# Kernel optimization log

Measured on AMD Instinct MI355X. Metric: run time of the kernel, lower is better.

Reference implementation:

```python
import jax, jax.numpy as jnp
from jax import lax
import numpy as np

TAU = 1.0          # epoch buffer = 0 -> tau_init * decay^0 = 1.0
NEG = -1.0e9
K_HOP = 2
MAX_CLUSTERS = 16
SIZE_MAX = 8
SIZE_MIN = 1
THRESH = 0.95
EPS = 1e-8


def _gumbel_hard(key, logits, m):
    # torch: logits*mask + (1-mask)*-1e9; gumbel noise; softmax; straight-through one-hot
    mf = m.astype(logits.dtype)
    ml = logits * mf + (1.0 - mf) * NEG
    u = jax.random.uniform(key, logits.shape, dtype=logits.dtype)
    g = -jnp.log(-jnp.log(u + EPS) + EPS)
    soft = jax.nn.softmax((ml + g) / TAU, axis=-1)
    idx = jnp.argmax(soft, axis=-1)
    hard = jax.nn.one_hot(idx, logits.shape[-1], dtype=logits.dtype)
    return hard + soft - lax.stop_gradient(soft), idx


def _k_hop(adj, seed_idx, m):
    # vectorized BFS via masked bmm, fixed K_HOP iterations
    N = adj.shape[1]
    seed = jax.nn.one_hot(seed_idx, N, dtype=bool)
    reach, cur = seed, seed
    for _ in range(K_HOP):
        nb = (jnp.einsum('bn,bnm->bm', cur.astype(adj.dtype), adj) > 0) & m
        new = nb & (~reach)
        reach = reach | nb
        cur = new
    return reach


def _topk_gumbel(key, logits, k, m):
    # iterative hard gumbel selection of up to k nodes per batch (k: [B] int)
    sel = jnp.zeros_like(logits)
    remaining = m
    for step in range(SIZE_MAX - SIZE_MIN):
        key, sk = jax.random.split(key)
        active = (step < k) & remaining.any(-1)
        step_mask = remaining & active[:, None]
        s, _ = _gumbel_hard(sk, logits, step_mask)
        sel = sel + s * active[:, None].astype(sel.dtype)
        remaining = remaining & ~(lax.stop_gradient(s) > 0.5)
    return sel


def _gru_seq(hist, h0, Wih, Whh, bih, bhh):
    # torch nn.GRU cell math, scan over time; hist [B,T,D], h0 [B,H]
    H = h0.shape[-1]
    def step(h, xt):
        gi = xt @ Wih.T + bih
        gh = h @ Whh.T + bhh
        r = jax.nn.sigmoid(gi[:, :H] + gh[:, :H])
        z = jax.nn.sigmoid(gi[:, H:2 * H] + gh[:, H:2 * H])
        n = jnp.tanh(gi[:, 2 * H:] + r * gh[:, 2 * H:])
        return (1.0 - z) * n + z * h, None
    h_final, _ = lax.scan(step, h0, jnp.swapaxes(hist, 0, 1))
    return h_final


def _forward(x, adj, mask, sel_w1, sel_b1, sel_w2, sel_b2,
             size_w1, size_b1, size_w2, size_b2,
             gru_wih, gru_whh, gru_bih, gru_bhh, init_w, init_b):
    B, N, D = x.shape
    H = init_w.shape[0]
    maskf = mask.astype(x.dtype)
    total = maskf.sum(-1)                                   # [B]
    x_mean = (x * maskf[:, :, None]).sum(1) / (total[:, None] + EPS)
    ctx_hidden = x_mean @ init_w.T + init_b                 # [B,H]
    global_ctx = ctx_hidden
    assignment = jnp.zeros((B, N, MAX_CLUSTERS), x.dtype)
    assigned = jnp.zeros((B, N), bool)
    history = []
    key = jax.random.key(42)
    size_range = jnp.arange(SIZE_MAX - SIZE_MIN + 1)
    for c in range(MAX_CLUSTERS):
        # gradient-safe early termination: mask contributions instead of breaking
        pct = assignment.sum((1, 2)) / (total + EPS)
        active = (pct < THRESH) & (total > 0)
        avail = mask & (~assigned)
        # selection MLP on [x, context]
        sel_in = jnp.concatenate(
            [x, jnp.broadcast_to(global_ctx[:, None, :], (B, N, H))], -1)
        h1 = jax.nn.relu(sel_in @ sel_w1.T + sel_b1)
        logits = (h1 @ sel_w2.T + sel_b2)[..., 0]           # [B,N]
        key, k1, k2, k3 = jax.random.split(key, 4)
        seed_sel, seed_idx = _gumbel_hard(k1, logits, avail)
        seed_feat = jnp.einsum('bn,bnd->bd', seed_sel, x)
        khop = _k_hop(adj, seed_idx, avail)
        candidates = khop & avail
        max_possible = jnp.minimum(candidates.sum(-1), SIZE_MAX)
        # cluster-size prediction
        size_in = jnp.concatenate(
            [seed_feat, global_ctx, max_possible.astype(x.dtype)[:, None]], -1)
        sh = jax.nn.relu(size_in @ size_w1.T + size_b1)
        size_logits = sh @ size_w2.T + size_b2              # [B,8]
        valid_ranges = jnp.clip(max_possible - SIZE_MIN + 1, 1, size_logits.shape[-1])
        range_mask = size_range[None, :] < valid_ranges[:, None]
        size_sel, _ = _gumbel_hard(k2, size_logits, range_mask)
        sizes = jnp.argmax(size_sel, -1) + SIZE_MIN         # [B]
        seed_oh = jax.nn.one_hot(seed_idx, N, dtype=bool)
        extra = _topk_gumbel(k3, logits, sizes - 1, candidates & (~seed_oh))
        cluster_sel = (seed_sel + extra) * active.astype(x.dtype)[:, None]
        assignment = assignment.at[:, :, c].set(cluster_sel)
        assigned = assigned | (lax.stop_gradient(cluster_sel) > 0.5)
        # gradient-safe cluster embedding (mean over selected nodes)
        csize = jnp.maximum(lax.stop_gradient(cluster_sel).sum(-1), 1.0)
        emb = jnp.einsum('bn,bnd->bd', cluster_sel, x) / csize[:, None]
        emb = emb * active.astype(x.dtype)[:, None]
        history.append(emb)
        # update_context_safe: rerun GRU on full history from current hidden
        hist = jnp.stack(history, 1)                        # [B,t+1,D]
        ctx_hidden = _gru_seq(hist, ctx_hidden, gru_wih, gru_whh, gru_bih, gru_bhh)
        global_ctx = ctx_hidden
    return assignment


def setup_inputs() -> dict:
    key = jax.random.key(0)
    ks = jax.random.split(key, 16)
    B, N, D, H = 32, 512, 128, 128
    x = jax.random.normal(ks[0], (B, N, D), jnp.float32)
    a = (jax.random.uniform(ks[1], (B, N, N)) < 0.02).astype(jnp.float32)
    adj = jnp.maximum(a, jnp.swapaxes(a, 1, 2))             # symmetric binary contacts
    mask = jnp.ones((B, N), bool)
    s = 0.05
    p = lambda k, sh: jax.random.normal(k, sh, jnp.float32) * s
    return dict(
        x=x, adj=adj, mask=mask,
        sel_w1=p(ks[2], (H, D + H)), sel_b1=p(ks[3], (H,)),
        sel_w2=p(ks[4], (1, H)), sel_b2=p(ks[5], (1,)),
        size_w1=p(ks[6], (H, D + H + 1)), size_b1=p(ks[7], (H,)),
        size_w2=p(ks[8], (SIZE_MAX, H)), size_b2=p(ks[9], (SIZE_MAX,)),
        gru_wih=p(ks[10], (3 * H, D)), gru_whh=p(ks[11], (3 * H, H)),
        gru_bih=p(ks[12], (3 * H,)), gru_bhh=p(ks[13], (3 * H,)),
        init_w=p(ks[14], (H, D)), init_b=p(ks[15], (H,)))


def reference(x, adj, mask, sel_w1, sel_b1, sel_w2, sel_b2,
              size_w1, size_b1, size_w2, size_b2,
              gru_wih, gru_whh, gru_bih, gru_bhh, init_w, init_b):
    return _forward(x, adj, mask, sel_w1, sel_b1, sel_w2, sel_b2,
                    size_w1, size_b1, size_w2, size_b2,
                    gru_wih, gru_whh, gru_bih, gru_bhh, init_w, init_b)
```

## Files before the change

kernel.cpp:

```cpp
#include <hip/hip_runtime.h>
#include <stdint.h>


#define NBATCH 32
#define NNODE  512
#define NDIM   128
#define NHID   128
#define NCLUS  16
#define NEGV   (-1.0e9f)
#define EPSF   (1e-8f)

struct KeyPack {
  uint32_t k1[NCLUS][2];
  uint32_t k2[NCLUS][2];
  uint32_t sk[NCLUS][7][2];
};

__host__ __device__ inline void tf2x32(uint32_t k0, uint32_t k1,
                                       uint32_t x0, uint32_t x1,
                                       uint32_t& o0, uint32_t& o1) {
  uint32_t k2 = k0 ^ k1 ^ 0x1BD11BDAu;
#define TFR(r) { x0 += x1; x1 = (x1 << (r)) | (x1 >> (32 - (r))); x1 ^= x0; }
  x0 += k0; x1 += k1;
  TFR(13) TFR(15) TFR(26) TFR(6)
  x0 += k1; x1 += k2 + 1u;
  TFR(17) TFR(29) TFR(16) TFR(24)
  x0 += k2; x1 += k0 + 2u;
  TFR(13) TFR(15) TFR(26) TFR(6)
  x0 += k0; x1 += k1 + 3u;
  TFR(17) TFR(29) TFR(16) TFR(24)
  x0 += k1; x1 += k2 + 4u;
  TFR(13) TFR(15) TFR(26) TFR(6)
  x0 += k2; x1 += k0 + 5u;
#undef TFR
  o0 = x0; o1 = x1;
}

__device__ __forceinline__ float jax_uniform(uint32_t k0, uint32_t k1, uint32_t j) {
  uint32_t a, b;
  tf2x32(k0, k1, 0u, j, a, b);
  uint32_t bits = a ^ b;
  return __uint_as_float((bits >> 9) | 0x3F800000u) - 1.0f;
}

__device__ __forceinline__ float gumb(float u) {
  return -logf(-logf(u + EPSF) + EPSF);
}

__device__ __forceinline__ float sigmf(float v) { return 1.0f / (1.0f + expf(-v)); }


__global__ void k_transpose(const float* __restrict__ gwih,
                            const float* __restrict__ gwhh,
                            const float* __restrict__ selw1, const float* __restrict__ szw1,
                            const float* __restrict__ initw,
                            float4* __restrict__ Wi3, float4* __restrict__ W3,
                            float* __restrict__ W1cT, float* __restrict__ szW1T,
                            float* __restrict__ initWT) {
  int t = blockIdx.x * blockDim.x + threadIdx.x;
  if (t < 32 * 384) {
    int i = t % 384, j4 = t / 384;
    const float* si = gwih + i * 128 + j4 * 4;
    Wi3[t] = make_float4(si[0], si[1], si[2], si[3]);
    const float* sh = gwhh + i * 128 + j4 * 4;
    W3[t]  = make_float4(sh[0], sh[1], sh[2], sh[3]);
  }
  if (t < 128 * 128) {
    int j = t >> 7, hh = t & 127;
    W1cT[t]   = selw1[hh * 256 + 128 + j];
    initWT[t] = initw[hh * 128 + j];
  }
  if (t < 257 * 128) {
    int j = t >> 7, i = t & 127;
    szW1T[t] = szw1[i * 257 + j];
  }
}

__global__ void k_adjbits(const float* __restrict__ adj, uint8_t* __restrict__ adjb8) {
  int t = blockIdx.x * blockDim.x + threadIdx.x;
  if (t >= NBATCH * NNODE * 64) return;
  const float4* p = (const float4*)adj + (size_t)t * 2;
  float4 a = p[0], b = p[1];
  uint32_t m = (a.x > 0.f ? 1u : 0u) | (a.y > 0.f ? 2u : 0u)
             | (a.z > 0.f ? 4u : 0u) | (a.w > 0.f ? 8u : 0u)
             | (b.x > 0.f ? 16u : 0u) | (b.y > 0.f ? 32u : 0u)
             | (b.z > 0.f ? 64u : 0u) | (b.w > 0.f ? 128u : 0u);
  adjb8[t] = (uint8_t)m;
}

__global__ __launch_bounds__(512)
void k_xw1(const float* __restrict__ x, const float* __restrict__ selw1,
           float* __restrict__ xw1T) {
  const int b = blockIdx.x >> 3;
  const int n0 = (blockIdx.x & 7) * 64;
  __shared__ float xs[64][NDIM + 1];
  for (int i = threadIdx.x; i < 64 * NDIM; i += 512) {
    int n = i >> 7, d = i & 127;
    xs[n][d] = x[((size_t)b * NNODE + n0 + n) * NDIM + d];
  }
  __syncthreads();
  for (int p = threadIdx.x; p < 64 * NHID; p += 512) {
    int h = p >> 6, n = p & 63;
    const float* wr = selw1 + h * 256;
    float a0 = 0.f, a1 = 0.f, a2 = 0.f, a3 = 0.f;
#pragma unroll 8
    for (int d = 0; d < NDIM; d += 4) {
      a0 = fmaf(xs[n][d + 0], wr[d + 0], a0);
      a1 = fmaf(xs[n][d + 1], wr[d + 1], a1);
      a2 = fmaf(xs[n][d + 2], wr[d + 2], a2);
      a3 = fmaf(xs[n][d + 3], wr[d + 3], a3);
    }
    xw1T[((size_t)b * NHID + h) * NNODE + n0 + n] = (a0 + a1) + (a2 + a3);
  }
}


#define MV384_PARTIALS(WP4, V4, PART)                                        \
  {                                                                          \
    const float4 cv0 = (V4)[wid * 4 + 0], cv1 = (V4)[wid * 4 + 1];           \
    const float4 cv2 = (V4)[wid * 4 + 2], cv3 = (V4)[wid * 4 + 3];           \
    _Pragma("unroll")                                                        \
    for (int m = 0; m < 6; m++) {                                            \
      const int row = lane + 64 * m;                                         \
      float4 w0 = (WP4)[row], w1 = (WP4)[384 + row];                         \
      float4 w2 = (WP4)[768 + row], w3v = (WP4)[1152 + row];                 \
      float pa = w0.x * cv0.x, pb = w0.y * cv0.y;                            \
      pa = fmaf(w0.z, cv0.z, pa);  pb = fmaf(w0.w, cv0.w, pb);               \
      pa = fmaf(w1.x, cv1.x, pa);  pb = fmaf(w1.y, cv1.y, pb);               \
      pa = fmaf(w1.z, cv1.z, pa);  pb = fmaf(w1.w, cv1.w, pb);               \
      pa = fmaf(w2.x, cv2.x, pa);  pb = fmaf(w2.y, cv2.y, pb);               \
      pa = fmaf(w2.z, cv2.z, pa);  pb = fmaf(w2.w, cv2.w, pb);               \
      pa = fmaf(w3v.x, cv3.x, pa); pb = fmaf(w3v.y, cv3.y, pb);              \
      pa = fmaf(w3v.z, cv3.z, pa); pb = fmaf(w3v.w, cv3.w, pb);              \
      (PART)[wid * 384 + row] = pa + pb;                                     \
    }                                                                        \
  }

__global__ __launch_bounds__(512)
void k_main(const float* __restrict__ x,
            const float* __restrict__ selb1, const float* __restrict__ selw2,
            const float* __restrict__ selb2,
            const float* __restrict__ szb1, const float* __restrict__ szw2,
            const float* __restrict__ szb2,
            const float* __restrict__ gbih, const float* __restrict__ gbhh,
            const float* __restrict__ initb,
            const float* __restrict__ xw1T, const uint32_t* __restrict__ adjb,
            const float4* __restrict__ Wi3, const float4* __restrict__ W3,
            const float* __restrict__ W1cT, const float* __restrict__ szW1T,
            const float* __restrict__ initWT,
            float* __restrict__ out, KeyPack kp)
{
  const int b = blockIdx.x;
  const int t = threadIdx.x;
  const int lane = t & 63, wid = t >> 6;

  __shared__ __align__(16) float4 resW[6144];
  __shared__ __align__(16) float gic[NCLUS][3 * NHID];
  __shared__ __align__(16) float partf[6144];
  __shared__ __align__(16) float gbhh_s[384];
  __shared__ __align__(16) float ctxb[NHID];
  __shared__ __align__(16) float ctxterm[NHID];
  __shared__ __align__(16) float cat256[2 * NHID];
  __shared__ __align__(16) float embs[NDIM];
  __shared__ __align__(16) float h1s[NHID];
  __shared__ __align__(16) float xm[NHID];
  __shared__ __align__(16) float selw2s[NHID];
  __shared__ float slog[8];
  __shared__ int   ibox[4];
  __shared__ uint32_t availw[16];
  __shared__ uint32_t curm[16];
  __shared__ uint32_t selm[16];

#pragma unroll
  for (int i = 0; i < 12; i++) {
    int idx = i * 512 + t;
    int dch = idx / 384, row = idx % 384;
    int sj4 = 4 * (dch >> 1) + (dch & 1);
    resW[idx] = W3[(size_t)sj4 * 384 + row];
  }
  if (t < 384) gbhh_s[t] = gbhh[t];
  if (t < NHID) selw2s[t] = selw2[t];
  const float selb2_r = selb2[0];
  const float szb2_r  = szb2[wid];
  const float selb1_r = (t < NHID) ? selb1[t] : 0.f;
  const float szb1_r  = (t < NHID) ? szb1[t] : 0.f;
  const float szw1mp_r = (t < NHID) ? szW1T[256 * NHID + t] : 0.f;
  const float gbih_r  = (t < 384) ? gbih[t] : 0.f;

  {
    const int j = t & 127, p = t >> 7;
    const float* xp = x + ((size_t)b * NNODE + p * 128) * NDIM + j;
    float a0 = 0.f, a1 = 0.f, a2 = 0.f, a3 = 0.f;
#pragma unroll 4
    for (int n = 0; n < 128; n += 4) {
      a0 += xp[(size_t)(n + 0) * NDIM];
      a1 += xp[(size_t)(n + 1) * NDIM];
      a2 += xp[(size_t)(n + 2) * NDIM];
      a3 += xp[(size_t)(n + 3) * NDIM];
    }
    partf[p * 128 + j] = (a0 + a1) + (a2 + a3);
  }
  __syncthreads();
  if (t < NHID) xm[t] = (partf[t] + partf[128 + t] + partf[256 + t] + partf[384 + t]) * (1.0f / 512.0f);
  __syncthreads();
  if (t < NHID) {
    float a = initb[t];
    const float4* x4 = (const float4*)xm;
#pragma unroll 8
    for (int j4 = 0; j4 < 32; j4++) {
      float4 v = x4[j4];
      int j = 4 * j4;
      a = fmaf(v.x, initWT[(j + 0) * NHID + t], a);
      a = fmaf(v.y, initWT[(j + 1) * NHID + t], a);
      a = fmaf(v.z, initWT[(j + 2) * NHID + t], a);
      a = fmaf(v.w, initWT[(j + 3) * NHID + t], a);
    }
    ctxb[t] = a;
  }
  __syncthreads();

  bool assigned = false;
  uint32_t selbits = 0u;

  for (int c = 0; c < NCLUS; c++) {
    {
      const int hh = t & 127, p = t >> 7;
      const float4* c4 = (const float4*)(ctxb + p * 32);
      float a0 = 0.f, a1 = 0.f, a2 = 0.f, a3 = 0.f;
#pragma unroll
      for (int j4 = 0; j4 < 8; j4++) {
        float4 cv = c4[j4];
        int j = p * 32 + j4 * 4;
        a0 = fmaf(cv.x, W1cT[(j + 0) * NHID + hh], a0);
        a1 = fmaf(cv.y, W1cT[(j + 1) * NHID + hh], a1);
        a2 = fmaf(cv.z, W1cT[(j + 2) * NHID + hh], a2);
        a3 = fmaf(cv.w, W1cT[(j + 3) * NHID + hh], a3);
      }
      partf[p * 128 + hh] = (a0 + a1) + (a2 + a3);
    }
    __syncthreads();
    if (t < NHID) ctxterm[t] = selb1_r + partf[t] + partf[128 + t] + partf[256 + t] + partf[384 + t];
    __syncthreads();

    float myLogit;
    {
      float acc0 = selb2_r, acc1 = 0.f, acc2 = 0.f, acc3 = 0.f;
      const float* xp = xw1T + (size_t)b * NHID * NNODE + t;
      const float4* ct4 = (const float4*)ctxterm;
      const float4* w24 = (const float4*)selw2s;
#pragma unroll 8
      for (int h4 = 0; h4 < 32; h4++) {
        float4 cv = ct4[h4], wv = w24[h4];
        int h = h4 * 4;
        acc0 = fmaf(fmaxf(xp[(size_t)(h + 0) * NNODE] + cv.x, 0.f), wv.x, acc0);
        acc1 = fmaf(fmaxf(xp[(size_t)(h + 1) * NNODE] + cv.y, 0.f), wv.y, acc1);
        acc2 = fmaf(fmaxf(xp[(size_t)(h + 2) * NNODE] + cv.z, 0.f), wv.z, acc2);
        acc3 = fmaf(fmaxf(xp[(size_t)(h + 3) * NNODE] + cv.w, 0.f), wv.w, acc3);
      }
      myLogit = (acc0 + acc1) + (acc2 + acc3);
    }
    {
      const bool avail = !assigned;
      float z = (avail ? myLogit : NEGV)
              + gumb(jax_uniform(kp.k1[c][0], kp.k1[c][1], (uint32_t)(b * NNODE + t)));
      partf[t] = z;
      partf[4096 + t] = myLogit;
#pragma unroll
      for (int s = 0; s < 7; s++)
        partf[512 + s * 512 + t] =
            gumb(jax_uniform(kp.sk[c][s][0], kp.sk[c][s][1], (uint32_t)(b * NNODE + t)));
      unsigned long long ab = __ballot(!assigned);
      if (lane == 0) { availw[2 * wid] = (uint32_t)ab; availw[2 * wid + 1] = (uint32_t)(ab >> 32); }
    }
    __syncthreads();

    if (wid == 0) {
      float bv = -3.4e38f; int bi = 0x7fffffff;
#pragma unroll
      for (int k = 0; k < 8; k++) {
        float v = partf[lane + 64 * k];
        if (v > bv) { bv = v; bi = lane + 64 * k; }
      }
#pragma unroll
      for (int off = 32; off > 0; off >>= 1) {
        float ov = __shfl_down(bv, off); int oi = __shfl_down(bi, off);
        if (ov > bv || (ov == bv && oi < bi)) { bv = ov; bi = oi; }
      }
      const int seed = __shfl(bi, 0);
      const float cf0 = x[((size_t)b * NNODE + seed) * NDIM + lane];
      const float cf1 = x[((size_t)b * NNODE + seed) * NDIM + 64 + lane];

      uint32_t av[16], reach[16], cw[16];
#pragma unroll
      for (int k = 0; k < 16; k++) av[k] = availw[k];
#pragma unroll
      for (int k = 0; k < 16; k++) {
        uint32_t s0 = ((seed >> 5) == k) ? (1u << (seed & 31)) : 0u;
        reach[k] = s0; cw[k] = s0;
      }
#pragma unroll
      for (int hop = 0; hop < 2; hop++) {
        uint32_t carrier = 0u;
#pragma unroll
        for (int k = 0; k < 16; k++) carrier = (lane == k) ? cw[k] : carrier;
        uint32_t myw = __shfl(carrier, lane >> 2);
        uint32_t mybyte = (myw >> ((lane & 3) * 8)) & 0xffu;
        uint32_t acc[16];
#pragma unroll
        for (int k = 0; k < 16; k++) acc[k] = 0u;
        while (mybyte) {
          int b2 = __ffs(mybyte) - 1; mybyte &= mybyte - 1;
          const uint4* r4 = (const uint4*)(adjb + ((size_t)b * NNODE + 8 * lane + b2) * 16);
          uint4 q0 = r4[0], q1 = r4[1], q2 = r4[2], q3 = r4[3];
          acc[0] |= q0.x; acc[1] |= q0.y; acc[2]  |= q0.z; acc[3]  |= q0.w;
          acc[4] |= q1.x; acc[5] |= q1.y; acc[6]  |= q1.z; acc[7]  |= q1.w;
          acc[8] |= q2.x; acc[9] |= q2.y; acc[10] |= q2.z; acc[11] |= q2.w;
          acc[12] |= q3.x; acc[13] |= q3.y; acc[14] |= q3.z; acc[15] |= q3.w;
        }
#pragma unroll
        for (int off = 1; off < 64; off <<= 1) {
#pragma unroll
          for (int k = 0; k < 16; k++) acc[k] |= __shfl_xor(acc[k], off);
        }
#pragma unroll
        for (int k = 0; k < 16; k++) {
          uint32_t nb = acc[k] & av[k];
          uint32_t nw = nb & ~reach[k];
          reach[k] |= nb;
          cw[k] = nw;
        }
      }
      int cnt = 0;
#pragma unroll
      for (int k = 0; k < 16; k++) cnt += __popc(reach[k]);
      if (lane == 0) {
        ibox[0] = seed; ibox[1] = min(cnt, 8); ibox[3] = cnt;
#pragma unroll
        for (int k = 0; k < 16; k++) curm[k] = reach[k];
      }
      cat256[lane] = cf0;
      cat256[64 + lane] = cf1;
    } else if (wid == 1) {
      cat256[NHID + lane] = ctxb[lane];
      cat256[NHID + 64 + lane] = ctxb[64 + lane];
    }
    __syncthreads();
    const int mp = ibox[1];

    {
      const int hh = t & 127, p = t >> 7;
      const float4* c4 = (const float4*)(cat256 + p * 64);
      float a0 = 0.f, a1 = 0.f, a2 = 0.f, a3 = 0.f;
#pragma unroll
      for (int j4 = 0; j4 < 16; j4++) {
        float4 cv = c4[j4];
        int j = p * 64 + j4 * 4;
        a0 = fmaf(cv.x, szW1T[(j + 0) * NHID + hh], a0);
        a1 = fmaf(cv.y, szW1T[(j + 1) * NHID + hh], a1);
        a2 = fmaf(cv.z, szW1T[(j + 2) * NHID + hh], a2);
        a3 = fmaf(cv.w, szW1T[(j + 3) * NHID + hh], a3);
      }
      partf[p * 128 + hh] = (a0 + a1) + (a2 + a3);
    }
    __syncthreads();
    if (t < NHID) {
      float a = szb1_r + ((partf[t] + partf[128 + t]) + (partf[256 + t] + partf[384 + t]))
              + (float)mp * szw1mp_r;
      h1s[t] = fmaxf(a, 0.f);
    }
    __syncthreads();
    {
      float a = h1s[lane] * szw2[wid * NHID + lane]
              + h1s[64 + lane] * szw2[wid * NHID + 64 + lane];
#pragma unroll
      for (int off = 32; off > 0; off >>= 1) a += __shfl_down(a, off);
      if (lane == 0) {
        float g2 = gumb(jax_uniform(kp.k2[c][0], kp.k2[c][1], (uint32_t)(b * 8 + wid)));
        slog[wid] = ((wid < mp) ? (a + szb2_r) : NEGV) + g2;
      }
    }
    __syncthreads();

    if (wid == 0) {
      float bv0 = slog[0]; int kextra = 0;
#pragma unroll
      for (int q = 1; q < 8; q++) if (slog[q] > bv0) { bv0 = slog[q]; kextra = q; }
      const int seed = ibox[0];
      uint32_t sw[16], remw[16];
#pragma unroll
      for (int k = 0; k < 16; k++) {
        uint32_t cwv = curm[k];
        uint32_t sb = ((seed >> 5) == k) ? (1u << (seed & 31)) : 0u;
        sw[k] = sb;
        remw[k] = cwv & ~sb;
      }
      int remcnt = ibox[3] - 1;
      int selcnt = 1;
      for (int s = 0; s < kextra; s++) {
        if (remcnt <= 0) break;
        uint32_t carrier = 0u;
#pragma unroll
        for (int k = 0; k < 16; k++) carrier = (lane == k) ? remw[k] : carrier;
        uint32_t myw = __shfl(carrier, lane >> 2);
        uint32_t mybyte = (myw >> ((lane & 3) * 8)) & 0xffu;
        float bv = -3.4e38f; int bi = 0x7fffffff;
#pragma unroll
        for (int b2 = 0; b2 < 8; b2++) {
          int n = 8 * lane + b2;
          float g  = partf[512 + s * 512 + n];
          float lg = partf[4096 + n];
          float v = ((mybyte >> b2) & 1u) ? (lg + g) : (NEGV + g);
          if (v > bv) { bv = v; bi = n; }
        }
#pragma unroll
        for (int off = 32; off > 0; off >>= 1) {
          float ov = __shfl_down(bv, off); int oi = __shfl_down(bi, off);
          if (ov > bv || (ov == bv && oi < bi)) { bv = ov; bi = oi; }
        }
        const int pick = __shfl(bi, 0);
#pragma unroll
        for (int k = 0; k < 16; k++) {
          uint32_t bit = ((pick >> 5) == k) ? (1u << (pick & 31)) : 0u;
          sw[k] |= bit;
          remw[k] &= ~bit;
        }
        remcnt--; selcnt++;
      }
      if (lane == 0) {
#pragma unroll
        for (int k = 0; k < 16; k++) selm[k] = sw[k];
        ibox[2] = selcnt;
      }
    }
    __syncthreads();

    {
      const bool sel = ((selm[t >> 5] >> (t & 31)) & 1u) != 0u;
      if (sel) selbits |= (1u << c);
      assigned = assigned || sel;
    }
    if (t < NDIM) {
      float a = 0.f;
      for (int w = 0; w < 16; w++) {
        uint32_t mwd = selm[w];
        while (mwd) {
          int bit = __ffs(mwd) - 1;
          mwd &= mwd - 1;
          a += x[((size_t)b * NNODE + (w * 32 + bit)) * NDIM + t];
        }
      }
      embs[t] = a / (float)ibox[2];
    }
    __syncthreads();

    {
      uintptr_t wp = (uintptr_t)Wi3;
      asm volatile("" : "+s"(wp));
      const float4* wi = (const float4*)wp + (size_t)wid * 4 * 384;
      const float4* e4 = (const float4*)embs;
      MV384_PARTIALS(wi, e4, partf)
    }
    __syncthreads();
    if (t < 384) {
      gic[c][t] = gbih_r
                + (((partf[t] + partf[384 + t]) + (partf[768 + t] + partf[1152 + t]))
                 + ((partf[1536 + t] + partf[1920 + t]) + (partf[2304 + t] + partf[2688 + t])));
    }
    __syncthreads();

    {
      const float4* cb4 = (const float4*)ctxb;
      float4 cv0 = cb4[wid * 4 + 0], cv1 = cb4[wid * 4 + 1];
      float4 cv2 = cb4[wid * 4 + 2], cv3 = cb4[wid * 4 + 3];
      for (int tt = 0; tt <= c; tt++) {
        float* pdst = partf + ((tt & 1) ? 3072 : 0);
        {
          uintptr_t gwp = (uintptr_t)W3;
          asm volatile("" : "+s"(gwp));
          const float4* ws = (const float4*)gwp;
#pragma unroll
          for (int m = 0; m < 6; m++) {
            const int row = lane + 64 * m;
            float4 w0 = resW[(2 * wid + 0) * 384 + row];
            float4 w1 = resW[(2 * wid + 1) * 384 + row];
            float4 w2 = ws[(size_t)(4 * wid + 2) * 384 + row];
            float4 w3v = ws[(size_t)(4 * wid + 3) * 384 + row];
            float pa = w0.x * cv0.x, pb = w0.y * cv0.y;
            pa = fmaf(w0.z, cv0.z, pa);  pb = fmaf(w0.w, cv0.w, pb);
            pa = fmaf(w1.x, cv1.x, pa);  pb = fmaf(w1.y, cv1.y, pb);
            pa = fmaf(w1.z, cv1.z, pa);  pb = fmaf(w1.w, cv1.w, pb);
            pa = fmaf(w2.x, cv2.x, pa);  pb = fmaf(w2.y, cv2.y, pb);
            pa = fmaf(w2.z, cv2.z, pa);  pb = fmaf(w2.w, cv2.w, pb);
            pa = fmaf(w3v.x, cv3.x, pa); pb = fmaf(w3v.y, cv3.y, pb);
            pa = fmaf(w3v.z, cv3.z, pa); pb = fmaf(w3v.w, cv3.w, pb);
            pdst[wid * 384 + row] = pa + pb;
          }
        }
        __syncthreads();
        float nv = 0.f;
        if (lane < 16) {
          const int u = 16 * wid + lane;
          const float* pp = partf + ((tt & 1) ? 3072 : 0);
          float ghr = ((pp[u]        + pp[384 + u])  + (pp[768 + u]  + pp[1152 + u]))
                    + ((pp[1536 + u] + pp[1920 + u]) + (pp[2304 + u] + pp[2688 + u]));
          float ghz = ((pp[128 + u]  + pp[512 + u])  + (pp[896 + u]  + pp[1280 + u]))
                    + ((pp[1664 + u] + pp[2048 + u]) + (pp[2432 + u] + pp[2816 + u]));
          float ghn = ((pp[256 + u]  + pp[640 + u])  + (pp[1024 + u] + pp[1408 + u]))
                    + ((pp[1792 + u] + pp[2176 + u]) + (pp[2560 + u] + pp[2944 + u]));
          const float* gi = gic[tt];
          float r  = sigmf(gi[u] + ghr + gbhh_s[u]);
          float zz = sigmf(gi[NHID + u] + ghz + gbhh_s[NHID + u]);
          float nn = tanhf(gi[2 * NHID + u] + r * (ghn + gbhh_s[2 * NHID + u]));
          float4 cc = (lane & 8) ? ((lane & 4) ? cv3 : cv2) : ((lane & 4) ? cv1 : cv0);
          float old = (lane & 2) ? ((lane & 1) ? cc.w : cc.z) : ((lane & 1) ? cc.y : cc.x);
          nv = (1.f - zz) * nn + zz * old;
        }
        if (tt == c) {
          if (lane < 16) ctxb[16 * wid + lane] = nv;
        } else {
          cv0 = make_float4(__shfl(nv, 0),  __shfl(nv, 1),  __shfl(nv, 2),  __shfl(nv, 3));
          cv1 = make_float4(__shfl(nv, 4),  __shfl(nv, 5),  __shfl(nv, 6),  __shfl(nv, 7));
          cv2 = make_float4(__shfl(nv, 8),  __shfl(nv, 9),  __shfl(nv, 10), __shfl(nv, 11));
          cv3 = make_float4(__shfl(nv, 12), __shfl(nv, 13), __shfl(nv, 14), __shfl(nv, 15));
        }
      }
    }
    __syncthreads();
  }

  float4* o4 = (float4*)(out + ((size_t)b * NNODE + t) * NCLUS);
#pragma unroll
  for (int q = 0; q < 4; q++) {
    float4 v;
    v.x = (selbits >> (4 * q + 0)) & 1u ? 1.f : 0.f;
    v.y = (selbits >> (4 * q + 1)) & 1u ? 1.f : 0.f;
    v.z = (selbits >> (4 * q + 2)) & 1u ? 1.f : 0.f;
    v.w = (selbits >> (4 * q + 3)) & 1u ? 1.f : 0.f;
    o4[q] = v;
  }
}


extern "C" void kernel_launch(void* const* d_in, const int* in_sizes, int n_in,
                              void* d_out, int out_size, void* d_ws, size_t ws_size,
                              hipStream_t stream) {
  (void)in_sizes; (void)n_in; (void)out_size; (void)ws_size;

  const float* x     = (const float*)d_in[0];
  const float* adj   = (const float*)d_in[1];
  const float* selw1 = (const float*)d_in[3];
  const float* selb1 = (const float*)d_in[4];
  const float* selw2 = (const float*)d_in[5];
  const float* selb2 = (const float*)d_in[6];
  const float* szw1  = (const float*)d_in[7];
  const float* szb1  = (const float*)d_in[8];
  const float* szw2  = (const float*)d_in[9];
  const float* szb2  = (const float*)d_in[10];
  const float* gwih  = (const float*)d_in[11];
  const float* gwhh  = (const float*)d_in[12];
  const float* gbih  = (const float*)d_in[13];
  const float* gbhh  = (const float*)d_in[14];
  const float* initw = (const float*)d_in[15];
  const float* initb = (const float*)d_in[16];
  float* out = (float*)d_out;

  float*    xw1T   = (float*)d_ws;
  uint32_t* adjb   = (uint32_t*)(xw1T + (size_t)NBATCH * NHID * NNODE);
  float*    Wi3    = (float*)(adjb + (size_t)NBATCH * NNODE * 16);
  float*    W3     = Wi3 + 384 * 128;
  float*    W1cT   = W3 + 384 * 128;
  float*    szW1T  = W1cT + 128 * 128;
  float*    initWT = szW1T + 257 * 128;

  KeyPack kp;
  uint32_t kk0 = 0u, kk1 = 42u;
  for (int c = 0; c < NCLUS; c++) {
    uint32_t nk0, nk1, t0, t1, u0, u1;
    tf2x32(kk0, kk1, 0u, 0u, nk0, nk1);
    tf2x32(kk0, kk1, 0u, 1u, kp.k1[c][0], kp.k1[c][1]);
    tf2x32(kk0, kk1, 0u, 2u, kp.k2[c][0], kp.k2[c][1]);
    tf2x32(kk0, kk1, 0u, 3u, t0, t1);
    for (int s = 0; s < 7; s++) {
      tf2x32(t0, t1, 0u, 1u, kp.sk[c][s][0], kp.sk[c][s][1]);
      tf2x32(t0, t1, 0u, 0u, u0, u1);
      t0 = u0; t1 = u1;
    }
    kk0 = nk0; kk1 = nk1;
  }

  k_transpose<<<192, 256, 0, stream>>>(gwih, gwhh, selw1, szw1, initw,
                                       (float4*)Wi3, (float4*)W3,
                                       W1cT, szW1T, initWT);
  k_adjbits<<<(NBATCH * NNODE * 64) / 256, 256, 0, stream>>>(adj, (uint8_t*)adjb);
  k_xw1<<<NBATCH * 8, 512, 0, stream>>>(x, selw1, xw1T);
  k_main<<<NBATCH, 512, 0, stream>>>(x, selb1, selw2, selb2, szb1, szw2, szb2,
                                     gbih, gbhh, initb, xw1T, adjb,
                                     (const float4*)Wi3, (const float4*)W3,
                                     W1cT, szW1T, initWT, out, kp);
}
```

Measured before the change: 816.7 us.

## Register-cache GRU weights, ping-pong context buffer, fast sigmoid/tanh in recurrence

In the inner GRU replay loop, half of each wave's Whh slice now loads from global into registers once per cluster instead of on every time step. The hidden-state update is recomputed by the first 128 threads into a double-buffered context array, replacing the per-wave shuffle broadcast. This adds a second barrier per step. Sigmoid and tanh switch to __expf-based fast versions. Shared scratch for Gumbel noise and logits is reorganised so availability masking happens at the argmax, and the FMA order is permuted. The result may differ slightly numerically, and register pressure rises.

```diff
diff --git a/kernel.cpp b/kernel.cpp
--- a/kernel.cpp
+++ b/kernel.cpp
@@ -47,7 +47,15 @@
   return -logf(-logf(u + EPSF) + EPSF);
 }
 
-__device__ __forceinline__ float sigmf(float v) { return 1.0f / (1.0f + expf(-v)); }
+__device__ __forceinline__ float sigmf_fast(float v) {
+  return 1.0f / (1.0f + __expf(-v));
+}
+__device__ __forceinline__ float tanh_fast(float x) {
+  float ax = fabsf(x);
+  float e = __expf(-2.0f * ax);
+  float r = (1.0f - e) / (1.0f + e);
+  return copysignf(r, x);
+}
 
 
 __global__ void k_transpose(const float* __restrict__ gwih,
@@ -127,9 +135,9 @@
       float pa = w0.x * cv0.x, pb = w0.y * cv0.y;                            \
       pa = fmaf(w0.z, cv0.z, pa);  pb = fmaf(w0.w, cv0.w, pb);               \
       pa = fmaf(w1.x, cv1.x, pa);  pb = fmaf(w1.y, cv1.y, pb);               \
-      pa = fmaf(w1.z, cv1.z, pa);  pb = fmaf(w1.w, cv1.w, pb);               \
       pa = fmaf(w2.x, cv2.x, pa);  pb = fmaf(w2.y, cv2.y, pb);               \
       pa = fmaf(w2.z, cv2.z, pa);  pb = fmaf(w2.w, cv2.w, pb);               \
+      pa = fmaf(w1.z, cv1.z, pa);  pb = fmaf(w1.w, cv1.w, pb);               \
       pa = fmaf(w3v.x, cv3.x, pa); pb = fmaf(w3v.y, cv3.y, pb);              \
       pa = fmaf(w3v.z, cv3.z, pa); pb = fmaf(w3v.w, cv3.w, pb);              \
       (PART)[wid * 384 + row] = pa + pb;                                     \
@@ -156,14 +164,13 @@
 
   __shared__ __align__(16) float4 resW[6144];
   __shared__ __align__(16) float gic[NCLUS][3 * NHID];
-  __shared__ __align__(16) float partf[6144];
-  __shared__ __align__(16) float gbhh_s[384];
-  __shared__ __align__(16) float ctxb[NHID];
+  __shared__ __align__(16) float part[8 * 384];
+  __shared__ __align__(16) float selbuf[9 * 512];
+  __shared__ __align__(16) float ctxb[2][NHID];
   __shared__ __align__(16) float ctxterm[NHID];
   __shared__ __align__(16) float cat256[2 * NHID];
   __shared__ __align__(16) float embs[NDIM];
   __shared__ __align__(16) float h1s[NHID];
-  __shared__ __align__(16) float xm[NHID];
   __shared__ __align__(16) float selw2s[NHID];
   __shared__ float slog[8];
   __shared__ int   ibox[4];
@@ -174,11 +181,10 @@
 #pragma unroll
   for (int i = 0; i < 12; i++) {
     int idx = i * 512 + t;
-    int dch = idx / 384, row = idx % 384;
-    int sj4 = 4 * (dch >> 1) + (dch & 1);
-    resW[idx] = W3[(size_t)sj4 * 384 + row];
-  }
-  if (t < 384) gbhh_s[t] = gbhh[t];
+    int w = idx / 768, rem = idx % 768;
+    resW[idx] = W3[(size_t)(4 * w) * 384 + rem];
+  }
+
   if (t < NHID) selw2s[t] = selw2[t];
   const float selb2_r = selb2[0];
   const float szb2_r  = szb2[wid];
@@ -186,6 +192,8 @@
   const float szb1_r  = (t < NHID) ? szb1[t] : 0.f;
   const float szw1mp_r = (t < NHID) ? szW1T[256 * NHID + t] : 0.f;
   const float gbih_r  = (t < 384) ? gbih[t] : 0.f;
+  float gb0 = 0.f, gb1 = 0.f, gb2 = 0.f;
+  if (t < NHID) { gb0 = gbhh[t]; gb1 = gbhh[NHID + t]; gb2 = gbhh[2 * NHID + t]; }
 
   {
     const int j = t & 127, p = t >> 7;
@@ -198,14 +206,14 @@
       a2 += xp[(size_t)(n + 2) * NDIM];
       a3 += xp[(size_t)(n + 3) * NDIM];
     }
-    partf[p * 128 + j] = (a0 + a1) + (a2 + a3);
+    part[p * 128 + j] = (a0 + a1) + (a2 + a3);
   }
   __syncthreads();
-  if (t < NHID) xm[t] = (partf[t] + partf[128 + t] + partf[256 + t] + partf[384 + t]) * (1.0f / 512.0f);
+  if (t < NHID) embs[t] = (part[t] + part[128 + t] + part[256 + t] + part[384 + t]) * (1.0f / 512.0f);
   __syncthreads();
   if (t < NHID) {
     float a = initb[t];
-    const float4* x4 = (const float4*)xm;
+    const float4* x4 = (const float4*)embs;
 #pragma unroll 8
     for (int j4 = 0; j4 < 32; j4++) {
       float4 v = x4[j4];
@@ -215,17 +223,18 @@
       a = fmaf(v.z, initWT[(j + 2) * NHID + t], a);
       a = fmaf(v.w, initWT[(j + 3) * NHID + t], a);
     }
-    ctxb[t] = a;
+    ctxb[0][t] = a;
   }
   __syncthreads();
 
+  int cur = 0;
   bool assigned = false;
   uint32_t selbits = 0u;
 
   for (int c = 0; c < NCLUS; c++) {
     {
       const int hh = t & 127, p = t >> 7;
-      const float4* c4 = (const float4*)(ctxb + p * 32);
+      const float4* c4 = (const float4*)(ctxb[cur] + p * 32);
       float a0 = 0.f, a1 = 0.f, a2 = 0.f, a3 = 0.f;
 #pragma unroll
       for (int j4 = 0; j4 < 8; j4++) {
@@ -236,13 +245,12 @@
         a2 = fmaf(cv.z, W1cT[(j + 2) * NHID + hh], a2);
         a3 = fmaf(cv.w, W1cT[(j + 3) * NHID + hh], a3);
       }
-      partf[p * 128 + hh] = (a0 + a1) + (a2 + a3);
-    }
-    __syncthreads();
-    if (t < NHID) ctxterm[t] = selb1_r + partf[t] + partf[128 + t] + partf[256 + t] + partf[384 + t];
-    __syncthreads();
-
-    float myLogit;
+      part[p * 128 + hh] = (a0 + a1) + (a2 + a3);
+    }
+    __syncthreads();
+    if (t < NHID) ctxterm[t] = selb1_r + part[t] + part[128 + t] + part[256 + t] + part[384 + t];
+    __syncthreads();
+
     {
       float acc0 = selb2_r, acc1 = 0.f, acc2 = 0.f, acc3 = 0.f;
       const float* xp = xw1T + (size_t)b * NHID * NNODE + t;
@@ -257,17 +265,11 @@
         acc2 = fmaf(fmaxf(xp[(size_t)(h + 2) * NNODE] + cv.z, 0.f), wv.z, acc2);
         acc3 = fmaf(fmaxf(xp[(size_t)(h + 3) * NNODE] + cv.w, 0.f), wv.w, acc3);
       }
-      myLogit = (acc0 + acc1) + (acc2 + acc3);
-    }
-    {
-      const bool avail = !assigned;
-      float z = (avail ? myLogit : NEGV)
-              + gumb(jax_uniform(kp.k1[c][0], kp.k1[c][1], (uint32_t)(b * NNODE + t)));
-      partf[t] = z;
-      partf[4096 + t] = myLogit;
+      selbuf[t] = (acc0 + acc1) + (acc2 + acc3);
+      selbuf[512 + t] = gumb(jax_uniform(kp.k1[c][0], kp.k1[c][1], (uint32_t)(b * NNODE + t)));
 #pragma unroll
       for (int s = 0; s < 7; s++)
-        partf[512 + s * 512 + t] =
+        selbuf[1024 + s * 512 + t] =
             gumb(jax_uniform(kp.sk[c][s][0], kp.sk[c][s][1], (uint32_t)(b * NNODE + t)));
       unsigned long long ab = __ballot(!assigned);
       if (lane == 0) { availw[2 * wid] = (uint32_t)ab; availw[2 * wid + 1] = (uint32_t)(ab >> 32); }
@@ -278,8 +280,10 @@
       float bv = -3.4e38f; int bi = 0x7fffffff;
 #pragma unroll
       for (int k = 0; k < 8; k++) {
-        float v = partf[lane + 64 * k];
-        if (v > bv) { bv = v; bi = lane + 64 * k; }
+        int n = lane + 64 * k;
+        bool av = (availw[n >> 5] >> (n & 31)) & 1u;
+        float v = (av ? selbuf[n] : NEGV) + selbuf[512 + n];
+        if (v > bv) { bv = v; bi = n; }
       }
 #pragma unroll
       for (int off = 32; off > 0; off >>= 1) {
@@ -341,8 +345,8 @@
       cat256[lane] = cf0;
       cat256[64 + lane] = cf1;
     } else if (wid == 1) {
-      cat256[NHID + lane] = ctxb[lane];
-      cat256[NHID + 64 + lane] = ctxb[64 + lane];
+      cat256[NHID + lane] = ctxb[cur][lane];
+      cat256[NHID + 64 + lane] = ctxb[cur][64 + lane];
     }
     __syncthreads();
     const int mp = ibox[1];
@@ -360,11 +364,11 @@
         a2 = fmaf(cv.z, szW1T[(j + 2) * NHID + hh], a2);
         a3 = fmaf(cv.w, szW1T[(j + 3) * NHID + hh], a3);
       }
-      partf[p * 128 + hh] = (a0 + a1) + (a2 + a3);
+      part[p * 128 + hh] = (a0 + a1) + (a2 + a3);
     }
     __syncthreads();
     if (t < NHID) {
-      float a = szb1_r + ((partf[t] + partf[128 + t]) + (partf[256 + t] + partf[384 + t]))
+      float a = szb1_r + ((part[t] + part[128 + t]) + (part[256 + t] + part[384 + t]))
               + (float)mp * szw1mp_r;
       h1s[t] = fmaxf(a, 0.f);
     }
@@ -407,8 +411,8 @@
 #pragma unroll
         for (int b2 = 0; b2 < 8; b2++) {
           int n = 8 * lane + b2;
-          float g  = partf[512 + s * 512 + n];
-          float lg = partf[4096 + n];
+          float g  = selbuf[1024 + s * 512 + n];
+          float lg = selbuf[n];
           float v = ((mybyte >> b2) & 1u) ? (lg + g) : (NEGV + g);
           if (v > bv) { bv = v; bi = n; }
         }
@@ -458,74 +462,67 @@
       asm volatile("" : "+s"(wp));
       const float4* wi = (const float4*)wp + (size_t)wid * 4 * 384;
       const float4* e4 = (const float4*)embs;
-      MV384_PARTIALS(wi, e4, partf)
+      MV384_PARTIALS(wi, e4, part)
     }
     __syncthreads();
     if (t < 384) {
       gic[c][t] = gbih_r
-                + (((partf[t] + partf[384 + t]) + (partf[768 + t] + partf[1152 + t]))
-                 + ((partf[1536 + t] + partf[1920 + t]) + (partf[2304 + t] + partf[2688 + t])));
-    }
-    __syncthreads();
-
-    {
-      const float4* cb4 = (const float4*)ctxb;
-      float4 cv0 = cb4[wid * 4 + 0], cv1 = cb4[wid * 4 + 1];
-      float4 cv2 = cb4[wid * 4 + 2], cv3 = cb4[wid * 4 + 3];
+                + (((part[t] + part[384 + t]) + (part[768 + t] + part[1152 + t]))
+                 + ((part[1536 + t] + part[1920 + t]) + (part[2304 + t] + part[2688 + t])));
+    }
+    __syncthreads();
+
+    {
+      uintptr_t gwp = (uintptr_t)W3;
+      asm volatile("" : "+s"(gwp));
+      const float4* ws = (const float4*)gwp;
+      float4 wreg[12];
+#pragma unroll
+      for (int m = 0; m < 6; m++) {
+        wreg[2 * m + 0] = ws[(size_t)(4 * wid + 2) * 384 + lane + 64 * m];
+        wreg[2 * m + 1] = ws[(size_t)(4 * wid + 3) * 384 + lane + 64 * m];
+      }
       for (int tt = 0; tt <= c; tt++) {
-        float* pdst = partf + ((tt & 1) ? 3072 : 0);
         {
-          uintptr_t gwp = (uintptr_t)W3;
-          asm volatile("" : "+s"(gwp));
-          const float4* ws = (const float4*)gwp;
+          const float4* c4 = (const float4*)ctxb[cur];
+          const float4 cv0 = c4[wid * 4 + 0], cv1 = c4[wid * 4 + 1];
+          const float4 cv2 = c4[wid * 4 + 2], cv3 = c4[wid * 4 + 3];
 #pragma unroll
           for (int m = 0; m < 6; m++) {
             const int row = lane + 64 * m;
-            float4 w0 = resW[(2 * wid + 0) * 384 + row];
-            float4 w1 = resW[(2 * wid + 1) * 384 + row];
-            float4 w2 = ws[(size_t)(4 * wid + 2) * 384 + row];
-            float4 w3v = ws[(size_t)(4 * wid + 3) * 384 + row];
+            float4 w2 = wreg[2 * m + 0];
+            float4 w3v = wreg[2 * m + 1];
+            float4 w0 = resW[wid * 768 + row];
+            float4 w1 = resW[wid * 768 + 384 + row];
             float pa = w0.x * cv0.x, pb = w0.y * cv0.y;
             pa = fmaf(w0.z, cv0.z, pa);  pb = fmaf(w0.w, cv0.w, pb);
             pa = fmaf(w1.x, cv1.x, pa);  pb = fmaf(w1.y, cv1.y, pb);
-            pa = fmaf(w1.z, cv1.z, pa);  pb = fmaf(w1.w, cv1.w, pb);
             pa = fmaf(w2.x, cv2.x, pa);  pb = fmaf(w2.y, cv2.y, pb);
             pa = fmaf(w2.z, cv2.z, pa);  pb = fmaf(w2.w, cv2.w, pb);
+            pa = fmaf(w1.z, cv1.z, pa);  pb = fmaf(w1.w, cv1.w, pb);
             pa = fmaf(w3v.x, cv3.x, pa); pb = fmaf(w3v.y, cv3.y, pb);
             pa = fmaf(w3v.z, cv3.z, pa); pb = fmaf(w3v.w, cv3.w, pb);
-            pdst[wid * 384 + row] = pa + pb;
+            part[wid * 384 + row] = pa + pb;
           }
         }
         __syncthreads();
-        float nv = 0.f;
-        if (lane < 16) {
-          const int u = 16 * wid + lane;
-          const float* pp = partf + ((tt & 1) ? 3072 : 0);
-          float ghr = ((pp[u]        + pp[384 + u])  + (pp[768 + u]  + pp[1152 + u]))
-                    + ((pp[1536 + u] + pp[1920 + u]) + (pp[2304 + u] + pp[2688 + u]));
-          float ghz = ((pp[128 + u]  + pp[512 + u])  + (pp[896 + u]  + pp[1280 + u]))
-                    + ((pp[1664 + u] + pp[2048 + u]) + (pp[2432 + u] + pp[2816 + u]));
-          float ghn = ((pp[256 + u]  + pp[640 + u])  + (pp[1024 + u] + pp[1408 + u]))
-                    + ((pp[1792 + u] + pp[2176 + u]) + (pp[2560 + u] + pp[2944 + u]));
+        if (t < NHID) {
+          float ghr = ((part[t]        + part[384 + t])  + (part[768 + t]  + part[1152 + t]))
+                    + ((part[1536 + t] + part[1920 + t]) + (part[2304 + t] + part[2688 + t]));
+          float ghz = ((part[128 + t]  + part[512 + t])  + (part[896 + t]  + part[1280 + t]))
+                    + ((part[1664 + t] + part[2048 + t]) + (part[2432 + t] + part[2816 + t]));
+          float ghn = ((part[256 + t]  + part[640 + t])  + (part[1024 + t] + part[1408 + t]))
+                    + ((part[1792 + t] + part[2176 + t]) + (part[2560 + t] + part[2944 + t]));
           const float* gi = gic[tt];
-          float r  = sigmf(gi[u] + ghr + gbhh_s[u]);
-          float zz = sigmf(gi[NHID + u] + ghz + gbhh_s[NHID + u]);
-          float nn = tanhf(gi[2 * NHID + u] + r * (ghn + gbhh_s[2 * NHID + u]));
-          float4 cc = (lane & 8) ? ((lane & 4) ? cv3 : cv2) : ((lane & 4) ? cv1 : cv0);
-          float old = (lane & 2) ? ((lane & 1) ? cc.w : cc.z) : ((lane & 1) ? cc.y : cc.x);
-          nv = (1.f - zz) * nn + zz * old;
-        }
-        if (tt == c) {
-          if (lane < 16) ctxb[16 * wid + lane] = nv;
-        } else {
-          cv0 = make_float4(__shfl(nv, 0),  __shfl(nv, 1),  __shfl(nv, 2),  __shfl(nv, 3));
-          cv1 = make_float4(__shfl(nv, 4),  __shfl(nv, 5),  __shfl(nv, 6),  __shfl(nv, 7));
-          cv2 = make_float4(__shfl(nv, 8),  __shfl(nv, 9),  __shfl(nv, 10), __shfl(nv, 11));
-          cv3 = make_float4(__shfl(nv, 12), __shfl(nv, 13), __shfl(nv, 14), __shfl(nv, 15));
-        }
-      }
-    }
-    __syncthreads();
+          float r  = sigmf_fast(gi[t] + ghr + gb0);
+          float zz = sigmf_fast(gi[NHID + t] + ghz + gb1);
+          float nn = tanh_fast(gi[2 * NHID + t] + r * (ghn + gb2));
+          ctxb[cur ^ 1][t] = (1.f - zz) * nn + zz * ctxb[cur][t];
+        }
+        __syncthreads();
+        cur ^= 1;
+      }
+    }
   }
 
   float4* o4 = (float4*)(out + ((size_t)b * NNODE + t) * NCLUS);
```

New measurement: 696.8 us. 14.7% less time.
